# Performance work log

Hardware: AMD Instinct MI355X
Metric: run time of the kernel (lower is better)

Reference implementation:

```python
import jax, jax.numpy as jnp
import numpy as np

B, S, IN, OUT, R, E = 8, 2048, 4096, 4096, 16, 64
ALPHA = 1.0


def setup_inputs() -> dict:
    ks = jax.random.split(jax.random.key(0), 7)
    return {
        "x": jax.random.normal(ks[0], (B, S, IN), jnp.float32),
        "query_signal": jax.random.normal(ks[1], (B, IN), jnp.float32),
        "A_pool": jax.random.normal(ks[2], (E, R, IN), jnp.float32),
        # original inits B pool to zeros; use small random values for a non-degenerate baseline
        "B_pool": jax.random.normal(ks[3], (E, OUT, R), jnp.float32) * 0.02,
        "W_rA": jax.random.normal(ks[4], (E, IN), jnp.float32) * 0.02,
        "b_rA": jnp.zeros((E,), jnp.float32),
        "W_rB": jax.random.normal(ks[5], (E, IN), jnp.float32) * 0.02,
        "b_rB": jnp.zeros((E,), jnp.float32),
        "cfs_W": jax.random.normal(ks[6], (R, IN, E), jnp.float32),
    }


def reference(x, query_signal, A_pool, B_pool, W_rA, b_rA, W_rB, b_rB, cfs_W):
    ranks = jnp.arange(R)  # rank slot k pairs with the k-th top-k expert index
    # IFS router A -> top-r expert indices per sample
    g_A_scores = query_signal @ W_rA.T + b_rA            # (B, E)
    _, idx_A = jax.lax.top_k(g_A_scores, R)              # (B, R)
    # gather: k-th selected expert contributes its k-th rank row
    lora_A = A_pool[idx_A, ranks[None, :], :]            # (B, R, IN)
    # router B scores: IFS linear + CFS content score (detached lora_A)
    g_B_scores = (query_signal @ W_rB.T + b_rB
                  + jnp.einsum('bri,rie->be', jax.lax.stop_gradient(lora_A), cfs_W))  # (B, E)
    _, idx_B = jax.lax.top_k(g_B_scores, R)              # (B, R)
    lora_B = jnp.transpose(B_pool, (0, 2, 1))[idx_B, ranks[None, :], :]  # (B, R, OUT)
    # two batched low-rank matmuls
    after_A = jnp.einsum('bsi,bri->bsr', x, lora_A)      # (B, S, R)
    lora_delta = jnp.einsum('bsr,bro->bso', after_A, lora_B)  # (B, S, OUT)
    return lora_delta * ALPHA
```

## Files before the change

kernel.cpp:

```cpp
#include <hip/hip_runtime.h>

#define B_ 8
#define S_ 2048
#define IN_ 4096
#define OUT_ 4096
#define R_ 16
#define E_ 64

typedef float v4f __attribute__((ext_vector_type(4)));

__device__ __forceinline__ float4 ntload4(const float* p) {
  v4f t = __builtin_nontemporal_load((const v4f*)p);
  float4 r; r.x = t.x; r.y = t.y; r.z = t.z; r.w = t.w; return r;
}
__device__ __forceinline__ void ntstore4(float* p, float4 v) {
  v4f t; t.x = v.x; t.y = v.y; t.z = v.z; t.w = v.w;
  __builtin_nontemporal_store(t, (v4f*)p);
}

__device__ __forceinline__ float dot4(float4 a, float4 b) {
  return a.x*b.x + a.y*b.y + a.z*b.z + a.w*b.w;
}

__device__ __forceinline__ void topk16(float v, int* __restrict__ dst) {
  const int lane = threadIdx.x & 63;
  for (int r = 0; r < R_; ++r) {
    float mv = v; int mi = lane;
    #pragma unroll
    for (int off = 1; off < 64; off <<= 1) {
      float v2 = __shfl_xor(mv, off, 64);
      int   i2 = __shfl_xor(mi, off, 64);
      if (v2 > mv || (v2 == mv && i2 < mi)) { mv = v2; mi = i2; }
    }
    if (lane == 0) dst[r] = mi;
    if (lane == mi) v = -__builtin_inff();
  }
}

__global__ __launch_bounds__(256) void k_scores(
    const float* __restrict__ q, const float* __restrict__ W_rA,
    const float* __restrict__ b_rA, const float* __restrict__ W_rB,
    const float* __restrict__ b_rB, float* __restrict__ scoresA,
    float* __restrict__ gB0)
{
  const int b = blockIdx.x >> 3, eg = blockIdx.x & 7;
  __shared__ float qs[IN_];
  const int tid = threadIdx.x;
  {
    const float4* q4 = (const float4*)(q + (size_t)b * IN_);
    float4* s4 = (float4*)qs;
    for (int i = tid; i < IN_ / 4; i += 256) s4[i] = q4[i];
  }
  __syncthreads();
  const int wave = tid >> 6, lane = tid & 63;
  const float4* qs4 = (const float4*)qs;
  for (int k = 0; k < 2; ++k) {
    const int e = eg * 8 + wave * 2 + k;
    const float4* wa = (const float4*)(W_rA + (size_t)e * IN_);
    const float4* wb = (const float4*)(W_rB + (size_t)e * IN_);
    float pa = 0.f, pb = 0.f;
    for (int i = lane; i < IN_ / 4; i += 64) {
      float4 qv = qs4[i];
      pa += dot4(qv, wa[i]);
      pb += dot4(qv, wb[i]);
    }
    #pragma unroll
    for (int off = 1; off < 64; off <<= 1) {
      pa += __shfl_xor(pa, off, 64);
      pb += __shfl_xor(pb, off, 64);
    }
    if (lane == 0) {
      scoresA[b * E_ + e] = pa + b_rA[e];
      gB0[b * E_ + e]     = pb + b_rB[e];
    }
  }
}

__global__ __launch_bounds__(64) void k_topk_a(
    const float* __restrict__ scoresA, int* __restrict__ idxA)
{
  const int b = blockIdx.x;
  topk16(scoresA[b * E_ + (threadIdx.x & 63)], idxA + b * R_);
}

__global__ __launch_bounds__(256) void k_cfs(
    const float* __restrict__ A_pool, const float* __restrict__ cfs,
    const int* __restrict__ idxA, float* __restrict__ gBpart)
{
  const int blk = blockIdx.x;
  const int r = blk >> 3, ic = blk & 7;
  __shared__ float as[B_][512];
  __shared__ float red[4][B_][E_];
  const int tid = threadIdx.x;
  {
    const int b = tid >> 5, t = tid & 31;
    const int e = idxA[b * R_ + r];
    const float4* src = (const float4*)(A_pool + ((size_t)e * R_ + r) * IN_ + ic * 512);
    float4* dst = (float4*)as[b];
    for (int j = t; j < 128; j += 32) dst[j] = src[j];
  }
  __syncthreads();
  const int e = tid & 63, part = tid >> 6;
  float acc[B_];
  #pragma unroll
  for (int b = 0; b < B_; ++b) acc[b] = 0.f;
  const float* cbase = cfs + ((size_t)r * IN_ + ic * 512) * E_ + e;
  for (int i = part * 128; i < part * 128 + 128; ++i) {
    float c = __builtin_nontemporal_load(cbase + (size_t)i * E_);
    #pragma unroll
    for (int b = 0; b < B_; ++b) acc[b] += as[b][i] * c;
  }
  #pragma unroll
  for (int b = 0; b < B_; ++b) red[part][b][e] = acc[b];
  __syncthreads();
  if (tid < 64) {
    #pragma unroll
    for (int b = 0; b < B_; ++b)
      gBpart[((size_t)blk * B_ + b) * E_ + tid] =
          red[0][b][tid] + red[1][b][tid] + red[2][b][tid] + red[3][b][tid];
  }
}

__global__ __launch_bounds__(64) void k_topk_b(
    const float* __restrict__ gB0, const float* __restrict__ gBpart,
    int* __restrict__ idxB)
{
  const int b = blockIdx.x;
  const int lane = threadIdx.x & 63;
  float v = gB0[b * E_ + lane];
  for (int blk = 0; blk < 128; ++blk)
    v += gBpart[((size_t)blk * B_ + b) * E_ + lane];
  topk16(v, idxB + b * R_);
}

__global__ __launch_bounds__(256) void k_pack_b(
    const float* __restrict__ B_pool, const int* __restrict__ idxB,
    float* __restrict__ loraBp)
{
  const int blk = blockIdx.x;
  const int b = blk >> 4, r = blk & 15;
  const int e = idxB[b * R_ + r];
  const float* src = B_pool + (size_t)e * OUT_ * R_ + r;
  float* dst = loraBp + (size_t)(b * R_ + r) * OUT_;
  for (int o = threadIdx.x; o < OUT_; o += 256) dst[o] = src[(size_t)o * R_];
}

__global__ __launch_bounds__(256) void k_after(
    const float* __restrict__ x, const float* __restrict__ A_pool,
    const int* __restrict__ idxA, float* __restrict__ partial)
{
  const int bx = blockIdx.x;
  const int rt = bx & 31, b = (bx >> 5) & 7, ks = bx >> 8;
  const int row0 = rt * 64;
  __shared__ float4 As[R_][128];
  __shared__ float aa[64][R_];
  const int tid = threadIdx.x;
  {
    const int sr = tid >> 4, st = tid & 15;
    const float4* src =
        (const float4*)(A_pool + ((size_t)idxA[b * R_ + sr] * R_ + sr) * IN_ + ks * 512);
    #pragma unroll
    for (int j = st; j < 128; j += 16) As[sr][j] = src[j];
  }
  const int rg = tid >> 4, p = tid & 15;
  const float* xbase = x + ((size_t)b * S_ + row0 + rg * 4) * IN_ + ks * 512;
  float acc[4][R_];
  #pragma unroll
  for (int m = 0; m < 4; ++m)
    #pragma unroll
    for (int r = 0; r < R_; ++r) acc[m][r] = 0.f;
  __syncthreads();

  #pragma unroll 2
  for (int step = 0; step < 8; ++step) {
    const int i4 = step * 16 + p;
    float4 xv[4];
    #pragma unroll
    for (int m = 0; m < 4; ++m)
      xv[m] = ntload4(xbase + (size_t)m * IN_ + i4 * 4);
    #pragma unroll
    for (int r = 0; r < R_; ++r) {
      float4 a = As[r][i4];
      #pragma unroll
      for (int m = 0; m < 4; ++m) acc[m][r] += dot4(xv[m], a);
    }
  }
  #pragma unroll
  for (int m = 0; m < 4; ++m)
    #pragma unroll
    for (int r = 0; r < R_; ++r) {
      float v = acc[m][r];
      v += __shfl_xor(v, 1, 64);
      v += __shfl_xor(v, 2, 64);
      v += __shfl_xor(v, 4, 64);
      v += __shfl_xor(v, 8, 64);
      acc[m][r] = v;
    }
  if (p == 0) {
    #pragma unroll
    for (int m = 0; m < 4; ++m) {
      float4* d4 = (float4*)aa[rg * 4 + m];
      d4[0] = make_float4(acc[m][0],  acc[m][1],  acc[m][2],  acc[m][3]);
      d4[1] = make_float4(acc[m][4],  acc[m][5],  acc[m][6],  acc[m][7]);
      d4[2] = make_float4(acc[m][8],  acc[m][9],  acc[m][10], acc[m][11]);
      d4[3] = make_float4(acc[m][12], acc[m][13], acc[m][14], acc[m][15]);
    }
  }
  __syncthreads();
  float4 w = ((const float4*)aa)[tid];
  *((float4*)(partial + (((size_t)ks * B_ + b) * S_ + row0) * R_) + tid) = w;
}

__global__ __launch_bounds__(256) void k_reduce(
    const float* __restrict__ partial, float* __restrict__ afterA)
{
  const int idx = blockIdx.x * 256 + threadIdx.x;
  const float4* p4 = (const float4*)partial;
  const size_t stride = (size_t)B_ * S_ * R_ / 4;
  float4 s = p4[idx];
  #pragma unroll
  for (int k = 1; k < 8; ++k) {
    float4 t = p4[(size_t)k * stride + idx];
    s.x += t.x; s.y += t.y; s.z += t.z; s.w += t.w;
  }
  ((float4*)afterA)[idx] = s;
}

__global__ __launch_bounds__(256) void k_out(
    const float* __restrict__ afterA, const float* __restrict__ loraBp,
    float* __restrict__ out)
{
  const int bx = blockIdx.x;
  const int b = bx >> 6, oc = (bx >> 4) & 3, st = bx & 15;
  __shared__ float aa[128 * R_];
  const int tid = threadIdx.x;
  {
    const float4* src = (const float4*)(afterA + ((size_t)b * S_ + st * 128) * R_);
    float4* aa4 = (float4*)aa;
    for (int j = tid; j < 512; j += 256) aa4[j] = src[j];
  }
  float4 Bf[R_];
  #pragma unroll
  for (int r = 0; r < R_; ++r)
    Bf[r] = *(const float4*)(loraBp + (size_t)(b * R_ + r) * OUT_ + oc * 1024 + tid * 4);
  __syncthreads();
  float* obase = out + ((size_t)b * S_ + st * 128) * OUT_ + oc * 1024 + tid * 4;
  #pragma unroll 2
  for (int s = 0; s < 128; ++s) {
    const float4* av = (const float4*)(aa + s * R_);
    float4 a0 = av[0], a1 = av[1], a2 = av[2], a3 = av[3];
    float4 o = make_float4(0.f, 0.f, 0.f, 0.f);
    o.x += a0.x*Bf[0].x;  o.y += a0.x*Bf[0].y;  o.z += a0.x*Bf[0].z;  o.w += a0.x*Bf[0].w;
    o.x += a0.y*Bf[1].x;  o.y += a0.y*Bf[1].y;  o.z += a0.y*Bf[1].z;  o.w += a0.y*Bf[1].w;
    o.x += a0.z*Bf[2].x;  o.y += a0.z*Bf[2].y;  o.z += a0.z*Bf[2].z;  o.w += a0.z*Bf[2].w;
    o.x += a0.w*Bf[3].x;  o.y += a0.w*Bf[3].y;  o.z += a0.w*Bf[3].z;  o.w += a0.w*Bf[3].w;
    o.x += a1.x*Bf[4].x;  o.y += a1.x*Bf[4].y;  o.z += a1.x*Bf[4].z;  o.w += a1.x*Bf[4].w;
    o.x += a1.y*Bf[5].x;  o.y += a1.y*Bf[5].y;  o.z += a1.y*Bf[5].z;  o.w += a1.y*Bf[5].w;
    o.x += a1.z*Bf[6].x;  o.y += a1.z*Bf[6].y;  o.z += a1.z*Bf[6].z;  o.w += a1.z*Bf[6].w;
    o.x += a1.w*Bf[7].x;  o.y += a1.w*Bf[7].y;  o.z += a1.w*Bf[7].z;  o.w += a1.w*Bf[7].w;
    o.x += a2.x*Bf[8].x;  o.y += a2.x*Bf[8].y;  o.z += a2.x*Bf[8].z;  o.w += a2.x*Bf[8].w;
    o.x += a2.y*Bf[9].x;  o.y += a2.y*Bf[9].y;  o.z += a2.y*Bf[9].z;  o.w += a2.y*Bf[9].w;
    o.x += a2.z*Bf[10].x; o.y += a2.z*Bf[10].y; o.z += a2.z*Bf[10].z; o.w += a2.z*Bf[10].w;
    o.x += a2.w*Bf[11].x; o.y += a2.w*Bf[11].y; o.z += a2.w*Bf[11].z; o.w += a2.w*Bf[11].w;
    o.x += a3.x*Bf[12].x; o.y += a3.x*Bf[12].y; o.z += a3.x*Bf[12].z; o.w += a3.x*Bf[12].w;
    o.x += a3.y*Bf[13].x; o.y += a3.y*Bf[13].y; o.z += a3.y*Bf[13].z; o.w += a3.y*Bf[13].w;
    o.x += a3.z*Bf[14].x; o.y += a3.z*Bf[14].y; o.z += a3.z*Bf[14].z; o.w += a3.z*Bf[14].w;
    o.x += a3.w*Bf[15].x; o.y += a3.w*Bf[15].y; o.z += a3.w*Bf[15].z; o.w += a3.w*Bf[15].w;
    ntstore4(obase + (size_t)s * OUT_, o);
  }
}

extern "C" void kernel_launch(void* const* d_in, const int* in_sizes, int n_in,
                              void* d_out, int out_size, void* d_ws, size_t ws_size,
                              hipStream_t stream) {
  const float* x      = (const float*)d_in[0];
  const float* qsig   = (const float*)d_in[1];
  const float* A_pool = (const float*)d_in[2];
  const float* B_pool = (const float*)d_in[3];
  const float* W_rA   = (const float*)d_in[4];
  const float* b_rA   = (const float*)d_in[5];
  const float* W_rB   = (const float*)d_in[6];
  const float* b_rB   = (const float*)d_in[7];
  const float* cfs_W  = (const float*)d_in[8];
  float* out = (float*)d_out;

  char* w = (char*)d_ws;
  int*   idxA    = (int*)(w);
  int*   idxB    = (int*)(w + 512);
  float* scoresA = (float*)(w + 1024);
  float* gB0     = (float*)(w + 3072);
  float* gBpart  = (float*)(w + 5120);
  float* loraBp  = (float*)(w + 267264);
  float* partial = (float*)(w + 2364416);
  float* afterA  = (float*)(w + 19141632);

  k_scores<<<64, 256, 0, stream>>>(qsig, W_rA, b_rA, W_rB, b_rB, scoresA, gB0);
  k_topk_a<<<8, 64, 0, stream>>>(scoresA, idxA);
  k_cfs<<<128, 256, 0, stream>>>(A_pool, cfs_W, idxA, gBpart);
  k_topk_b<<<8, 64, 0, stream>>>(gB0, gBpart, idxB);
  k_pack_b<<<128, 256, 0, stream>>>(B_pool, idxB, loraBp);
  k_after<<<2048, 256, 0, stream>>>(x, A_pool, idxA, partial);
  k_reduce<<<256, 256, 0, stream>>>(partial, afterA);
  k_out<<<512, 256, 0, stream>>>(afterA, loraBp, out);
}
```

Measured before the change: 190.8 us.

## Fuse split-K reduction into output kernel and widen B-pack grid

Removes the separate k_reduce kernel. k_after now writes its split-K partials in a row-tile-major layout, so k_out can sum the 8 partials for its 32 rows directly into shared memory. k_out is retiled so each block covers 32 rows across all four output chunks, reloading the B registers per chunk. k_pack_b is split over four times as many blocks to spread the strided gather. Together these save a launch and a round-trip of the after_A buffer, at the cost of redundant B loads per block in k_out.

```diff
diff --git a/kernel.cpp b/kernel.cpp
--- a/kernel.cpp
+++ b/kernel.cpp
@@ -137,12 +137,16 @@
     const float* __restrict__ B_pool, const int* __restrict__ idxB,
     float* __restrict__ loraBp)
 {
-  const int blk = blockIdx.x;
-  const int b = blk >> 4, r = blk & 15;
+  const int bx = blockIdx.x;
+  const int b = bx >> 6, r = (bx >> 2) & 15, q = bx & 3;
   const int e = idxB[b * R_ + r];
   const float* src = B_pool + (size_t)e * OUT_ * R_ + r;
   float* dst = loraBp + (size_t)(b * R_ + r) * OUT_;
-  for (int o = threadIdx.x; o < OUT_; o += 256) dst[o] = src[(size_t)o * R_];
+  #pragma unroll
+  for (int i = 0; i < 4; ++i) {
+    const int o = q * 1024 + i * 256 + threadIdx.x;
+    dst[o] = src[(size_t)o * R_];
+  }
 }
 
 __global__ __launch_bounds__(256) void k_after(
@@ -208,65 +212,59 @@
   }
   __syncthreads();
   float4 w = ((const float4*)aa)[tid];
-  *((float4*)(partial + (((size_t)ks * B_ + b) * S_ + row0) * R_) + tid) = w;
-}
-
-__global__ __launch_bounds__(256) void k_reduce(
-    const float* __restrict__ partial, float* __restrict__ afterA)
-{
-  const int idx = blockIdx.x * 256 + threadIdx.x;
-  const float4* p4 = (const float4*)partial;
-  const size_t stride = (size_t)B_ * S_ * R_ / 4;
-  float4 s = p4[idx];
-  #pragma unroll
-  for (int k = 1; k < 8; ++k) {
-    float4 t = p4[(size_t)k * stride + idx];
-    s.x += t.x; s.y += t.y; s.z += t.z; s.w += t.w;
-  }
-  ((float4*)afterA)[idx] = s;
+  ntstore4(partial + (((size_t)(b * 32 + rt) * 8 + ks) << 10) + tid * 4, w);
 }
 
 __global__ __launch_bounds__(256) void k_out(
-    const float* __restrict__ afterA, const float* __restrict__ loraBp,
+    const float* __restrict__ partial, const float* __restrict__ loraBp,
     float* __restrict__ out)
 {
   const int bx = blockIdx.x;
-  const int b = bx >> 6, oc = (bx >> 4) & 3, st = bx & 15;
-  __shared__ float aa[128 * R_];
+  const int b = bx >> 6, st = bx & 63;
+  __shared__ float aa[32][R_];
   const int tid = threadIdx.x;
-  {
-    const float4* src = (const float4*)(afterA + ((size_t)b * S_ + st * 128) * R_);
-    float4* aa4 = (float4*)aa;
-    for (int j = tid; j < 512; j += 256) aa4[j] = src[j];
-  }
-  float4 Bf[R_];
-  #pragma unroll
-  for (int r = 0; r < R_; ++r)
-    Bf[r] = *(const float4*)(loraBp + (size_t)(b * R_ + r) * OUT_ + oc * 1024 + tid * 4);
-  __syncthreads();
-  float* obase = out + ((size_t)b * S_ + st * 128) * OUT_ + oc * 1024 + tid * 4;
-  #pragma unroll 2
-  for (int s = 0; s < 128; ++s) {
-    const float4* av = (const float4*)(aa + s * R_);
-    float4 a0 = av[0], a1 = av[1], a2 = av[2], a3 = av[3];
-    float4 o = make_float4(0.f, 0.f, 0.f, 0.f);
-    o.x += a0.x*Bf[0].x;  o.y += a0.x*Bf[0].y;  o.z += a0.x*Bf[0].z;  o.w += a0.x*Bf[0].w;
-    o.x += a0.y*Bf[1].x;  o.y += a0.y*Bf[1].y;  o.z += a0.y*Bf[1].z;  o.w += a0.y*Bf[1].w;
-    o.x += a0.z*Bf[2].x;  o.y += a0.z*Bf[2].y;  o.z += a0.z*Bf[2].z;  o.w += a0.z*Bf[2].w;
-    o.x += a0.w*Bf[3].x;  o.y += a0.w*Bf[3].y;  o.z += a0.w*Bf[3].z;  o.w += a0.w*Bf[3].w;
-    o.x += a1.x*Bf[4].x;  o.y += a1.x*Bf[4].y;  o.z += a1.x*Bf[4].z;  o.w += a1.x*Bf[4].w;
-    o.x += a1.y*Bf[5].x;  o.y += a1.y*Bf[5].y;  o.z += a1.y*Bf[5].z;  o.w += a1.y*Bf[5].w;
-    o.x += a1.z*Bf[6].x;  o.y += a1.z*Bf[6].y;  o.z += a1.z*Bf[6].z;  o.w += a1.z*Bf[6].w;
-    o.x += a1.w*Bf[7].x;  o.y += a1.w*Bf[7].y;  o.z += a1.w*Bf[7].z;  o.w += a1.w*Bf[7].w;
-    o.x += a2.x*Bf[8].x;  o.y += a2.x*Bf[8].y;  o.z += a2.x*Bf[8].z;  o.w += a2.x*Bf[8].w;
-    o.x += a2.y*Bf[9].x;  o.y += a2.y*Bf[9].y;  o.z += a2.y*Bf[9].z;  o.w += a2.y*Bf[9].w;
-    o.x += a2.z*Bf[10].x; o.y += a2.z*Bf[10].y; o.z += a2.z*Bf[10].z; o.w += a2.z*Bf[10].w;
-    o.x += a2.w*Bf[11].x; o.y += a2.w*Bf[11].y; o.z += a2.w*Bf[11].z; o.w += a2.w*Bf[11].w;
-    o.x += a3.x*Bf[12].x; o.y += a3.x*Bf[12].y; o.z += a3.x*Bf[12].z; o.w += a3.x*Bf[12].w;
-    o.x += a3.y*Bf[13].x; o.y += a3.y*Bf[13].y; o.z += a3.y*Bf[13].z; o.w += a3.y*Bf[13].w;
-    o.x += a3.z*Bf[14].x; o.y += a3.z*Bf[14].y; o.z += a3.z*Bf[14].z; o.w += a3.z*Bf[14].w;
-    o.x += a3.w*Bf[15].x; o.y += a3.w*Bf[15].y; o.z += a3.w*Bf[15].z; o.w += a3.w*Bf[15].w;
-    ntstore4(obase + (size_t)s * OUT_, o);
+  if (tid < 128) {
+    const float* base = partial + (((size_t)(b * 32 + (st >> 1)) * 8) << 10)
+                        + (st & 1) * 512 + tid * 4;
+    float4 s = ntload4(base);
+    #pragma unroll
+    for (int k = 1; k < 8; ++k) {
+      float4 t = ntload4(base + k * 1024);
+      s.x += t.x; s.y += t.y; s.z += t.z; s.w += t.w;
+    }
+    ((float4*)aa)[tid] = s;
+  }
+  __syncthreads();
+  const int row0 = st * 32;
+  for (int oc = 0; oc < 4; ++oc) {
+    float4 Bf[R_];
+    #pragma unroll
+    for (int r = 0; r < R_; ++r)
+      Bf[r] = *(const float4*)(loraBp + (size_t)(b * R_ + r) * OUT_ + oc * 1024 + tid * 4);
+    float* obase = out + ((size_t)b * S_ + row0) * OUT_ + oc * 1024 + tid * 4;
+    #pragma unroll 2
+    for (int s = 0; s < 32; ++s) {
+      const float4* av = (const float4*)aa[s];
+      float4 a0 = av[0], a1 = av[1], a2 = av[2], a3 = av[3];
+      float4 o = make_float4(0.f, 0.f, 0.f, 0.f);
+      o.x += a0.x*Bf[0].x;  o.y += a0.x*Bf[0].y;  o.z += a0.x*Bf[0].z;  o.w += a0.x*Bf[0].w;
+      o.x += a0.y*Bf[1].x;  o.y += a0.y*Bf[1].y;  o.z += a0.y*Bf[1].z;  o.w += a0.y*Bf[1].w;
+      o.x += a0.z*Bf[2].x;  o.y += a0.z*Bf[2].y;  o.z += a0.z*Bf[2].z;  o.w += a0.z*Bf[2].w;
+      o.x += a0.w*Bf[3].x;  o.y += a0.w*Bf[3].y;  o.z += a0.w*Bf[3].z;  o.w += a0.w*Bf[3].w;
+      o.x += a1.x*Bf[4].x;  o.y += a1.x*Bf[4].y;  o.z += a1.x*Bf[4].z;  o.w += a1.x*Bf[4].w;
+      o.x += a1.y*Bf[5].x;  o.y += a1.y*Bf[5].y;  o.z += a1.y*Bf[5].z;  o.w += a1.y*Bf[5].w;
+      o.x += a1.z*Bf[6].x;  o.y += a1.z*Bf[6].y;  o.z += a1.z*Bf[6].z;  o.w += a1.z*Bf[6].w;
+      o.x += a1.w*Bf[7].x;  o.y += a1.w*Bf[7].y;  o.z += a1.w*Bf[7].z;  o.w += a1.w*Bf[7].w;
+      o.x += a2.x*Bf[8].x;  o.y += a2.x*Bf[8].y;  o.z += a2.x*Bf[8].z;  o.w += a2.x*Bf[8].w;
+      o.x += a2.y*Bf[9].x;  o.y += a2.y*Bf[9].y;  o.z += a2.y*Bf[9].z;  o.w += a2.y*Bf[9].w;
+      o.x += a2.z*Bf[10].x; o.y += a2.z*Bf[10].y; o.z += a2.z*Bf[10].z; o.w += a2.z*Bf[10].w;
+      o.x += a2.w*Bf[11].x; o.y += a2.w*Bf[11].y; o.z += a2.w*Bf[11].z; o.w += a2.w*Bf[11].w;
+      o.x += a3.x*Bf[12].x; o.y += a3.x*Bf[12].y; o.z += a3.x*Bf[12].z; o.w += a3.x*Bf[12].w;
+      o.x += a3.y*Bf[13].x; o.y += a3.y*Bf[13].y; o.z += a3.y*Bf[13].z; o.w += a3.y*Bf[13].w;
+      o.x += a3.z*Bf[14].x; o.y += a3.z*Bf[14].y; o.z += a3.z*Bf[14].z; o.w += a3.z*Bf[14].w;
+      o.x += a3.w*Bf[15].x; o.y += a3.w*Bf[15].y; o.z += a3.w*Bf[15].z; o.w += a3.w*Bf[15].w;
+      ntstore4(obase + (size_t)s * OUT_, o);
+    }
   }
 }
 
@@ -292,14 +290,12 @@
   float* gBpart  = (float*)(w + 5120);
   float* loraBp  = (float*)(w + 267264);
   float* partial = (float*)(w + 2364416);
-  float* afterA  = (float*)(w + 19141632);
 
   k_scores<<<64, 256, 0, stream>>>(qsig, W_rA, b_rA, W_rB, b_rB, scoresA, gB0);
   k_topk_a<<<8, 64, 0, stream>>>(scoresA, idxA);
   k_cfs<<<128, 256, 0, stream>>>(A_pool, cfs_W, idxA, gBpart);
   k_topk_b<<<8, 64, 0, stream>>>(gB0, gBpart, idxB);
-  k_pack_b<<<128, 256, 0, stream>>>(B_pool, idxB, loraBp);
+  k_pack_b<<<512, 256, 0, stream>>>(B_pool, idxB, loraBp);
   k_after<<<2048, 256, 0, stream>>>(x, A_pool, idxA, partial);
-  k_reduce<<<256, 256, 0, stream>>>(partial, afterA);
-  k_out<<<512, 256, 0, stream>>>(afterA, loraBp, out);
-}
+  k_out<<<512, 256, 0, stream>>>(partial, loraBp, out);
+}
```

Result: no change. 193.5 us (+1.4%).
